# Kernel tuning notes

Hardware: AMD Instinct MI355X
Metric: run time of the kernel (lower is better)

The kernel has to match this reference:

```python
import jax, jax.numpy as jnp
import numpy as np

I3 = jnp.eye(3, dtype=jnp.float32)
G_VEC = jnp.array([0.0, 0.0, -9.80665], dtype=jnp.float32)
# Q diag: [cov_omega x3, cov_acc x3, cov_b_omega x3, cov_b_acc x3, cov_Rot_c_i x3, cov_t_c_i x3]
Q_DIAG = jnp.array([1e-3] * 3 + [1e-2] * 3 + [6e-9] * 3 + [2e-4] * 3 + [1e-9] * 3 + [1e-9] * 3, dtype=jnp.float32)
N_NORM_ROT = 100
N_NORM_ROT_CI = 1000


def skew(v):
    z = jnp.zeros_like(v[0])
    return jnp.stack([jnp.stack([z, -v[2], v[1]]),
                      jnp.stack([v[2], z, -v[0]]),
                      jnp.stack([-v[1], v[0], z])])


def so3exp(phi):
    a2 = jnp.sum(phi * phi)
    small = a2 < 1e-12
    a = jnp.sqrt(jnp.where(small, 1.0, a2))
    axis = phi / a
    c, s = jnp.cos(a), jnp.sin(a)
    big = c * I3 + (1.0 - c) * jnp.outer(axis, axis) + s * skew(axis)
    return jnp.where(small, I3 + skew(phi), big)


def sen3exp(xi):
    # SE_2(3) exponential: xi[:3]=rotation, xi[3:9]=(v, p) parts
    phi = xi[:3]
    a2 = jnp.sum(phi * phi)
    small = a2 < 1e-12
    a = jnp.sqrt(jnp.where(small, 1.0, a2))
    axis = phi / a
    c, s = jnp.cos(a), jnp.sin(a)
    sk = skew(axis)
    R = jnp.where(small, I3 + skew(phi),
                  c * I3 + (1.0 - c) * jnp.outer(axis, axis) + s * sk)
    J = jnp.where(small, I3 + 0.5 * skew(phi),
                  (s / a) * I3 + (1.0 - s / a) * jnp.outer(axis, axis) + ((1.0 - c) / a) * sk)
    x = J @ xi[3:].reshape(2, 3).T  # (3,2): columns are dv, dp
    return R, x


def normalize_rot(R):
    # Polar-factor re-orthonormalization (equivalent to the SVD-based
    # normalize_rot for near-rotation matrices), via Newton-Schulz iteration
    # which is smooth and jit/vjp friendly.
    def body(X, _):
        return 1.5 * X - 0.5 * (X @ X.T @ X), None
    X, _ = jax.lax.scan(body, R, None, length=8)
    return X


def from_rpy(roll, pitch, yaw):
    cr, sr = jnp.cos(roll), jnp.sin(roll)
    cp, sp = jnp.cos(pitch), jnp.sin(pitch)
    cy, sy = jnp.cos(yaw), jnp.sin(yaw)
    one = jnp.ones_like(cr)
    zero = jnp.zeros_like(cr)
    Rx = jnp.stack([jnp.stack([one, zero, zero]), jnp.stack([zero, cr, -sr]), jnp.stack([zero, sr, cr])])
    Ry = jnp.stack([jnp.stack([cp, zero, sp]), jnp.stack([zero, one, zero]), jnp.stack([-sp, zero, cp])])
    Rz = jnp.stack([jnp.stack([cy, -sy, zero]), jnp.stack([sy, cy, zero]), jnp.stack([zero, zero, one])])
    return Rz @ Ry @ Rx


def init_covariance():
    P = jnp.zeros((21, 21), dtype=jnp.float32)
    P = P.at[:2, :2].set(1e-3 * jnp.eye(2))     # cov_Rot0 (no yaw error)
    P = P.at[3:5, 3:5].set(0.1 * jnp.eye(2))    # cov_v0
    P = P.at[9:12, 9:12].set(6e-3 * I3)         # cov_b_omega0
    P = P.at[12:15, 12:15].set(4e-3 * I3)       # cov_b_acc0
    P = P.at[15:18, 15:18].set(1e-6 * I3)       # cov_Rot_c_i0
    P = P.at[18:21, 18:21].set(5e-3 * I3)       # cov_t_c_i0
    return P


def propagate_cov(P, Rot, v, p, dt):
    F = jnp.zeros((21, 21), dtype=P.dtype)
    F = F.at[3:6, :3].set(skew(G_VEC))
    F = F.at[6:9, 3:6].set(I3)
    F = F.at[:3, 9:12].set(-Rot)
    F = F.at[3:6, 9:12].set(-skew(v) @ Rot)
    F = F.at[3:6, 12:15].set(-Rot)
    F = F.at[6:9, 9:12].set(-skew(p) @ Rot)
    G = jnp.zeros((21, 18), dtype=P.dtype)
    G = G.at[:3, :3].set(Rot)
    G = G.at[3:6, 3:6].set(Rot)
    G = G.at[9:12, 6:9].set(I3)
    G = G.at[12:15, 9:12].set(I3)
    G = G.at[15:18, 12:15].set(I3)
    G = G.at[18:21, 15:18].set(I3)
    F = F * dt
    G = G * dt
    F2 = F @ F
    Phi = jnp.eye(21, dtype=P.dtype) + F + 0.5 * F2 + (F2 @ F) / 6.0  # 3rd-order expm
    return Phi @ (P + (G * Q_DIAG[None, :]) @ G.T) @ Phi.T


def _step(carry, xs):
    Rot, v, p, b_om, b_ac, Rci, tci, P = carry
    u_i, dt_i, mcov_i, i = xs
    # ---- propagate ----
    acc = Rot @ (u_i[3:6] - b_ac) + G_VEC
    v_n = v + acc * dt_i
    p_n = p + v * dt_i + 0.5 * acc * dt_i * dt_i
    Rot_n = Rot @ so3exp((u_i[:3] - b_om) * dt_i)
    P_n = propagate_cov(P, Rot, v, p, dt_i)
    # ---- update: zero lateral/vertical body-velocity pseudo-measurement ----
    omega = u_i[:3] - b_om
    Rot_body = Rot_n @ Rci
    v_imu = Rot_n.T @ v_n
    v_body = Rci.T @ v_imu + skew(tci) @ omega
    H = jnp.zeros((2, 21), dtype=P.dtype)
    H = H.at[:, 3:6].set(Rot_body.T[1:])
    H = H.at[:, 15:18].set((Rci.T @ skew(v_imu))[1:])
    H = H.at[:, 9:12].set(skew(tci)[1:])
    H = H.at[:, 18:21].set(-skew(omega)[1:])
    r = -v_body[1:]
    Rm = jnp.diag(mcov_i)
    S = H @ P_n @ H.T + Rm                    # (2,2)
    K = jnp.linalg.solve(S, H @ P_n).T        # K = P H^T S^-1 (P, S symmetric)
    dx = K @ r                                 # (21,)
    dR, dxi = sen3exp(dx[:9])
    Rot_u = dR @ Rot_n
    v_u = dR @ v_n + dxi[:, 0]
    p_u = dR @ p_n + dxi[:, 1]
    b_om_u = b_om + dx[9:12]
    b_ac_u = b_ac + dx[12:15]
    Rci_u = so3exp(dx[15:18]) @ Rci
    tci_u = tci + dx[18:21]
    IKH = jnp.eye(21, dtype=P.dtype) - K @ H
    P_u = IKH @ P_n @ IKH.T + K @ Rm @ K.T    # Joseph form
    P_u = 0.5 * (P_u + P_u.T)
    Rot_u = jnp.where(i % N_NORM_ROT == 0, normalize_rot(Rot_u), Rot_u)
    Rci_u = jnp.where(i % N_NORM_ROT_CI == 0, normalize_rot(Rci_u), Rci_u)
    carry = (Rot_u, v_u, p_u, b_om_u, b_ac_u, Rci_u, tci_u, P_u)
    return carry, (Rot_u, v_u, p_u, b_om_u, b_ac_u, Rci_u, tci_u)


def _forward(t, u, measurements_covs, v_mes, p_mes, ang0, N):
    dt = t[1:N] - t[:N - 1]
    Rot0 = from_rpy(ang0[0], ang0[1], ang0[2])
    z3 = jnp.zeros(3, dtype=u.dtype)
    carry0 = (Rot0, v_mes[0], z3, z3, z3, I3, z3, init_covariance())
    xs = (u[1:N], dt, measurements_covs[1:N], jnp.arange(1, N))
    _, ys = jax.lax.scan(_step, carry0, xs)
    Rot = jnp.concatenate([Rot0[None], ys[0]], axis=0)
    v = jnp.concatenate([v_mes[0][None], ys[1]], axis=0)
    p = jnp.concatenate([z3[None], ys[2]], axis=0)
    b_omega = jnp.concatenate([z3[None], ys[3]], axis=0)
    b_acc = jnp.concatenate([z3[None], ys[4]], axis=0)
    Rot_c_i = jnp.concatenate([I3[None], ys[5]], axis=0)
    t_c_i = jnp.concatenate([z3[None], ys[6]], axis=0)
    return (Rot, v, p, b_omega, b_acc, Rot_c_i, t_c_i)


def setup_inputs() -> dict:
    key = jax.random.key(0)
    N = 20000  # 200 s at 100 Hz IMU
    k0, k1, k2, k3, k4, k5 = jax.random.split(key, 6)
    t = jnp.arange(N, dtype=jnp.float32) * 0.01
    gyro = 0.01 * jax.random.normal(k0, (N, 3), dtype=jnp.float32)
    acc = jnp.array([0.0, 0.0, 9.80665], jnp.float32) + 0.1 * jax.random.normal(k1, (N, 3), dtype=jnp.float32)
    u = jnp.concatenate([gyro, acc], axis=1)
    measurements_covs = 0.1 + jax.random.uniform(k2, (N, 2), dtype=jnp.float32)
    v_mes = jax.random.normal(k3, (N, 3), dtype=jnp.float32)
    p_mes = jax.random.normal(k4, (N, 3), dtype=jnp.float32)
    ang0 = 0.01 * jax.random.normal(k5, (3,), dtype=jnp.float32)
    return dict(t=t, u=u, measurements_covs=measurements_covs, v_mes=v_mes, p_mes=p_mes, ang0=ang0, N=N)


def reference(t, u, measurements_covs, v_mes, p_mes, ang0, N):
    return _forward(t, u, measurements_covs, v_mes, p_mes, ang0, N)
```

## Files before the change

### kernel.cpp

```cpp
#include <hip/hip_runtime.h>

#define GRAV 9.80665f
#define WAVE_SYNC() do { \
    asm volatile("s_waitcnt lgkmcnt(0)" ::: "memory"); \
    __builtin_amdgcn_sched_barrier(0); \
  } while(0)

#define LDP 28

__device__ __forceinline__ float sel3(int r, float a0, float a1, float a2){
  float x = (r==1)? a1 : a0;
  return (r>=2)? a2 : x;
}
__device__ __forceinline__ float RL(float v, int k){
  return __int_as_float(__builtin_amdgcn_readlane(__float_as_int(v), k));
}
__device__ __forceinline__ float pick9(int k, const float* X){
  float s=X[0];
  s=(k==1)?X[1]:s; s=(k==2)?X[2]:s; s=(k==3)?X[3]:s; s=(k==4)?X[4]:s;
  s=(k==5)?X[5]:s; s=(k==6)?X[6]:s; s=(k==7)?X[7]:s; s=(k==8)?X[8]:s;
  return s;
}

__device__ __forceinline__ void mm33(float* __restrict__ O, const float* A, const float* B){
#pragma unroll
  for(int r=0;r<3;++r){
#pragma unroll
    for(int c=0;c<3;++c){
      O[r*3+c] = A[r*3+0]*B[0*3+c] + A[r*3+1]*B[1*3+c] + A[r*3+2]*B[2*3+c];
    }
  }
}

__device__ __forceinline__ void rot_from_t2(float t_, float p0, float p1, float p2, float* R){
  float c_, k1_, k2_;
  if (t_ < 1e-4f){
    c_  = 1.f - t_*(0.5f - t_*((1.f/24.f) - t_*(1.f/720.f)));
    k2_ = 1.f - t_*((1.f/6.f) - t_*((1.f/120.f) - t_*(1.f/5040.f)));
    k1_ = 0.5f - t_*((1.f/24.f) - t_*(1.f/720.f));
  } else {
    float a = sqrtf(t_);
    c_ = __cosf(a);
    float s = __sinf(a);
    k2_ = s/a;
    k1_ = (1.f - c_)/t_;
  }
  R[0]=c_+k1_*p0*p0;      R[1]=k1_*p0*p1-k2_*p2;  R[2]=k1_*p0*p2+k2_*p1;
  R[3]=k1_*p0*p1+k2_*p2;  R[4]=c_+k1_*p1*p1;      R[5]=k1_*p1*p2-k2_*p0;
  R[6]=k1_*p0*p2-k2_*p1;  R[7]=k1_*p1*p2+k2_*p0;  R[8]=c_+k1_*p2*p2;
}

__device__ __forceinline__ void normalize_rot9(float* X){
#pragma unroll 1
  for(int it=0; it<8; ++it){
    float Y[9], Z[9];
#pragma unroll
    for(int r=0;r<3;++r)
#pragma unroll
      for(int c=0;c<3;++c)
        Y[r*3+c] = X[r*3+0]*X[c*3+0] + X[r*3+1]*X[c*3+1] + X[r*3+2]*X[c*3+2];
#pragma unroll
    for(int r=0;r<3;++r)
#pragma unroll
      for(int c=0;c<3;++c)
        Z[r*3+c] = Y[r*3+0]*X[0*3+c] + Y[r*3+1]*X[1*3+c] + Y[r*3+2]*X[2*3+c];
#pragma unroll
    for(int e=0;e<9;++e) X[e] = 1.5f*X[e] - 0.5f*Z[e];
  }
}

__device__ __forceinline__ float pick_state(int l,
    const float* Rt, const float* vv, const float* pp,
    const float* bw, const float* ba, const float* Rc, const float* tc){
  float s = Rt[0];
  s=(l==1)?Rt[1]:s;  s=(l==2)?Rt[2]:s;  s=(l==3)?Rt[3]:s;  s=(l==4)?Rt[4]:s;
  s=(l==5)?Rt[5]:s;  s=(l==6)?Rt[6]:s;  s=(l==7)?Rt[7]:s;  s=(l==8)?Rt[8]:s;
  s=(l==9)?vv[0]:s;  s=(l==10)?vv[1]:s; s=(l==11)?vv[2]:s;
  s=(l==12)?pp[0]:s; s=(l==13)?pp[1]:s; s=(l==14)?pp[2]:s;
  s=(l==15)?bw[0]:s; s=(l==16)?bw[1]:s; s=(l==17)?bw[2]:s;
  s=(l==18)?ba[0]:s; s=(l==19)?ba[1]:s; s=(l==20)?ba[2]:s;
  s=(l==21)?Rc[0]:s; s=(l==22)?Rc[1]:s; s=(l==23)?Rc[2]:s;
  s=(l==24)?Rc[3]:s; s=(l==25)?Rc[4]:s; s=(l==26)?Rc[5]:s;
  s=(l==27)?Rc[6]:s; s=(l==28)?Rc[7]:s; s=(l==29)?Rc[8]:s;
  s=(l==30)?tc[0]:s; s=(l==31)?tc[1]:s; s=(l==32)?tc[2]:s;
  return s;
}

__global__ __launch_bounds__(64,1)
void iekf_scan_kernel(const float* __restrict__ t,
                      const float* __restrict__ u,
                      const float* __restrict__ mcov,
                      const float* __restrict__ v_mes,
                      const float* __restrict__ ang0,
                      float* __restrict__ out, int N)
{
  const int l = threadIdx.x;
  __shared__ __align__(16) float Pm[21*LDP];
  __shared__ __align__(16) float Eb[21*LDP];

  for (int e=l; e<21*LDP; e+=64){
    int r=e/LDP, c=e-(e/LDP)*LDP;
    float vI=0.f;
    if (r==c){
      if (r<2) vI=0.001f;
      else if (r==3||r==4) vI=0.1f;
      else if (r>=9&&r<12) vI=0.006f;
      else if (r>=12&&r<15) vI=0.004f;
      else if (r>=15&&r<18) vI=1e-6f;
      else if (r>=18&&r<21) vI=0.005f;
    }
    Pm[e]=vI;
  }

  int ostr=0; float* op = out;
  {
    int obase=0, ooff=0;
    if (l<9)       {obase=0;    ostr=9; ooff=l;}
    else if (l<12) {obase=9*N;  ostr=3; ooff=l-9;}
    else if (l<15) {obase=12*N; ostr=3; ooff=l-12;}
    else if (l<18) {obase=15*N; ostr=3; ooff=l-15;}
    else if (l<21) {obase=18*N; ostr=3; ooff=l-18;}
    else if (l<30) {obase=21*N; ostr=9; ooff=l-21;}
    else           {obase=30*N; ostr=3; ooff=l-30;}
    op = out + obase + ooff;
  }

  const int g21 = l/21;
  const int c21 = l - g21*21;
  const int cw  = 9 + 4*g21;
  int l1 = l+21; if (l1>=63) l1-=63;
  int l2 = l+42; if (l2>=63) l2-=63;
  static const int cols[12] = {3,4,5, 9,10,11, 15,16,17, 18,19,20};

  float myval = 0.f;
  {
    float Rt0[9], vv0[3], pp0[3], bwa[3], baa[3], Rc0[9], tca[3];
    float rl = ang0[0], pt = ang0[1], yw = ang0[2];
    float cr=cosf(rl), sr=sinf(rl), cp=cosf(pt), sp=sinf(pt), cy=cosf(yw), sy=sinf(yw);
    Rt0[0]=cy*cp; Rt0[1]=cy*sp*sr - sy*cr; Rt0[2]=cy*sp*cr + sy*sr;
    Rt0[3]=sy*cp; Rt0[4]=sy*sp*sr + cy*cr; Rt0[5]=sy*sp*cr - cy*sr;
    Rt0[6]=-sp;   Rt0[7]=cp*sr;            Rt0[8]=cp*cr;
    vv0[0]=v_mes[0]; vv0[1]=v_mes[1]; vv0[2]=v_mes[2];
#pragma unroll
    for(int k=0;k<3;++k){ pp0[k]=0.f; bwa[k]=0.f; baa[k]=0.f; tca[k]=0.f; }
    Rc0[0]=1.f;Rc0[1]=0.f;Rc0[2]=0.f;Rc0[3]=0.f;Rc0[4]=1.f;Rc0[5]=0.f;Rc0[6]=0.f;Rc0[7]=0.f;Rc0[8]=1.f;
    float sv = pick_state(l, Rt0, vv0, pp0, bwa, baa, Rc0, tca);
    if (l<33){ op[0] = sv; myval = sv; }
  }
  WAVE_SYNC();

  float tA = t[0], tB = t[1];
  float cu[6];
#pragma unroll
  for(int k=0;k<6;++k) cu[k]=u[6+k];
  float cm0=mcov[2], cm1=mcov[3];

  int nx100=100, nx1000=1000;

#pragma unroll 1
  for (int i=1; i<N; ++i){
    float dt = tB - tA;
    float u0=cu[0], u1=cu[1], u2=cu[2], u3=cu[3], u4=cu[4], u5=cu[5];
    float crm0=cm0, crm1=cm1;
    if (i+1 < N){
      tA = tB; tB = t[i+1];
#pragma unroll
      for(int k=0;k<6;++k) cu[k]=u[(i+1)*6+k];
      cm0 = mcov[(i+1)*2]; cm1 = mcov[(i+1)*2+1];
    }

    float Rt[9];
#pragma unroll
    for(int k=0;k<9;++k) Rt[k] = RL(myval, k);
    float vv0s=RL(myval,9),  vv1s=RL(myval,10), vv2s=RL(myval,11);
    float pp0s=RL(myval,12), pp1s=RL(myval,13), pp2s=RL(myval,14);
    float bw0=RL(myval,15),  bw1=RL(myval,16),  bw2=RL(myval,17);
    float ba0=RL(myval,18),  ba1=RL(myval,19),  ba2=RL(myval,20);
    float Rc[9];
#pragma unroll
    for(int k=0;k<9;++k) Rc[k] = RL(myval, 21+k);
    float tc0=RL(myval,30), tc1=RL(myval,31), tc2=RL(myval,32);

    float dt2=dt*dt, gdt=GRAV*dt, hdt=0.5f*dt, hdt2=0.5f*dt*dt;
    float hgdt2 = 0.5f*gdt*dt;
    float g6d   = gdt*dt2*(1.0f/6.0f);

    float w0=u0-bw0, w1=u1-bw1, w2=u2-bw2;
    float aa0=u3-ba0, aa1=u4-ba1, aa2=u5-ba2;
    float acc0 = Rt[0]*aa0+Rt[1]*aa1+Rt[2]*aa2;
    float acc1 = Rt[3]*aa0+Rt[4]*aa1+Rt[5]*aa2;
    float acc2 = Rt[6]*aa0+Rt[7]*aa1+Rt[8]*aa2 - GRAV;
    float vn0=vv0s+acc0*dt, vn1=vv1s+acc1*dt, vn2=vv2s+acc2*dt;
    float pn0=pp0s+vv0s*dt+acc0*hdt2;
    float pn1=pp1s+vv1s*dt+acc1*hdt2;
    float pn2=pp2s+vv2s*dt+acc2*hdt2;
    float ph0=w0*dt, ph1=w1*dt, ph2=w2*dt;
    float dRs[9]; rot_from_t2(ph0*ph0+ph1*ph1+ph2*ph2, ph0,ph1,ph2, dRs);
    float Rn[9]; mm33(Rn, Rt, dRs);

    float RtG[3], RtA[3], RtB[3];
#pragma unroll
    for(int k=0;k<3;++k){
      float r0=Rt[k], r3=Rt[3+k], r6=Rt[6+k];
      RtG[k] = sel3(g21, r0, r3, r6);
      RtA[k] = sel3(g21, r3, r6, r0);
      RtB[k] = sel3(g21, r6, r0, r3);
    }
    float vAs = sel3(g21, vv2s, vv0s, vv1s), vBs = sel3(g21, vv1s, vv2s, vv0s);
    float pAs = sel3(g21, pp2s, pp0s, pp1s), pBs = sel3(g21, pp1s, pp2s, pp0s);
    float Bs0,Bs1,Bs2, Cs0,Cs1,Cs2, Ds0,Ds1,Ds2;
    {
      float bs[3], cs[3], ds[3];
#pragma unroll
      for(int k=0;k<3;++k){
        bs[k] = -dt*RtG[k];
        float craw = dt*(vAs*RtA[k] - vBs*RtB[k]);
        float selC = sel3(g21, -RtA[k], RtB[k], 0.f);
        cs[k] = craw + hgdt2*selC;
        float draw = dt*(pAs*RtA[k] - pBs*RtB[k]);
        ds[k] = draw + hdt*craw + g6d*selC;
      }
      Bs0=bs[0];Bs1=bs[1];Bs2=bs[2];
      Cs0=cs[0];Cs1=cs[1];Cs2=cs[2];
      Ds0=ds[0];Ds1=ds[1];Ds2=ds[2];
    }

    float q0d=0.001f*dt2, q1d=0.01f*dt2;
    float q69=6e-9f*dt2, q24=2e-4f*dt2, q19=1e-9f*dt2;

    if (l<63){
      int c = c21;
      const float4* Pr4 = (const float4*)(Pm + c*LDP);
      float4 a0=Pr4[0], a1=Pr4[1], a2=Pr4[2], a3=Pr4[3], a4=Pr4[4];
      float m20 = Pm[c*LDP + 20];

      bool cl3 = (c<3);
      bool c36 = (c>=3 && c<6);
      int csel = c36 ? (c-3) : (cl3 ? c : 0);
      float Rtc0 = sel3(csel, Rt[0], Rt[3], Rt[6]);
      float Rtc1 = sel3(csel, Rt[1], Rt[4], Rt[7]);
      float Rtc2 = sel3(csel, Rt[2], Rt[5], Rt[8]);
      float dot0 = Rt[0]*Rtc0 + Rt[1]*Rtc1 + Rt[2]*Rtc2;
      float dot1 = Rt[3]*Rtc0 + Rt[4]*Rtc1 + Rt[5]*Rtc2;
      float dotg = RtG[0]*Rtc0 + RtG[1]*Rtc1 + RtG[2]*Rtc2;

      float m0  = a0.x + (cl3 ? q0d*dot0 : 0.f);
      float m1  = a0.y + (cl3 ? q0d*dot1 : 0.f);
      float mr  = sel3(g21, a0.x, a0.y, a0.z) + (cl3 ? q0d*dotg : 0.f);
      float m3r = sel3(g21, a0.w, a1.x, a1.y) + (c36 ? q1d*dotg : 0.f);
      float m6r = sel3(g21, a1.z, a1.w, a2.x);
      float m9  = a2.y + ((c==9) ? q69 : 0.f);
      float m10 = a2.z + ((c==10)? q69 : 0.f);
      float m11 = a2.w + ((c==11)? q69 : 0.f);
      float m12 = a3.x + ((c==12)? q24 : 0.f);
      float m13 = a3.y + ((c==13)? q24 : 0.f);
      float m14 = a3.z + ((c==14)? q24 : 0.f);

      float Ar = (g21==0)? gdt*m1 : (g21==1)? -gdt*m0 : 0.f;
      float bterm = Bs0*m12+Bs1*m13+Bs2*m14;
      float e0 = mr + Bs0*m9+Bs1*m10+Bs2*m11;
      float e1 = m3r + Ar + Cs0*m9+Cs1*m10+Cs2*m11 + bterm;
      float e2 = m6r + hdt*Ar + dt*m3r + Ds0*m9+Ds1*m10+Ds2*m11 + hdt*bterm;
      Eb[g21*LDP+c]=e0; Eb[(3+g21)*LDP+c]=e1; Eb[(6+g21)*LDP+c]=e2;

      float mc0 = sel3(g21, a2.y, a3.y, a4.y);
      float mc1 = sel3(g21, a2.z, a3.z, a4.z);
      float mc2 = sel3(g21, a2.w, a3.w, a4.w);
      float mc3 = sel3(g21, a3.x, a4.x, m20);
      float qd0 = sel3(g21, q69, q24, q19);
      float qd1 = sel3(g21, q69, q24, q19);
      float qd2 = sel3(g21, q69, q19, q19);
      float qd3 = sel3(g21, q24, q19, q19);
      Eb[(cw+0)*LDP+c] = mc0 + ((cw+0==c)? qd0 : 0.f);
      Eb[(cw+1)*LDP+c] = mc1 + ((cw+1==c)? qd1 : 0.f);
      Eb[(cw+2)*LDP+c] = mc2 + ((cw+2==c)? qd2 : 0.f);
      Eb[(cw+3)*LDP+c] = mc3 + ((cw+3==c)? qd3 : 0.f);
    }

    float H0[12], H1[12];
    float rr0, rr1;
    {
      float Rb1 = Rn[0]*Rc[1]+Rn[1]*Rc[4]+Rn[2]*Rc[7];
      float Rb4 = Rn[3]*Rc[1]+Rn[4]*Rc[4]+Rn[5]*Rc[7];
      float Rb7 = Rn[6]*Rc[1]+Rn[7]*Rc[4]+Rn[8]*Rc[7];
      float Rb2 = Rn[0]*Rc[2]+Rn[1]*Rc[5]+Rn[2]*Rc[8];
      float Rb5 = Rn[3]*Rc[2]+Rn[4]*Rc[5]+Rn[5]*Rc[8];
      float Rb8 = Rn[6]*Rc[2]+Rn[7]*Rc[5]+Rn[8]*Rc[8];
      float vi0 = Rn[0]*vn0+Rn[3]*vn1+Rn[6]*vn2;
      float vi1 = Rn[1]*vn0+Rn[4]*vn1+Rn[7]*vn2;
      float vi2 = Rn[2]*vn0+Rn[5]*vn1+Rn[8]*vn2;
      float vb1 = Rc[1]*vi0+Rc[4]*vi1+Rc[7]*vi2 + (tc2*w0 - tc0*w2);
      float vb2 = Rc[2]*vi0+Rc[5]*vi1+Rc[8]*vi2 + (tc0*w1 - tc1*w0);
      rr0 = -vb1; rr1 = -vb2;
      H0[0]=Rb1; H0[1]=Rb4; H0[2]=Rb7;
      H1[0]=Rb2; H1[1]=Rb5; H1[2]=Rb8;
      H0[3]=tc2;  H0[4]=0.f;  H0[5]=-tc0;
      H1[3]=-tc1; H1[4]=tc0;  H1[5]=0.f;
      H0[6]=Rc[4]*vi2 - Rc[7]*vi1;  H0[7]=Rc[7]*vi0 - Rc[1]*vi2;  H0[8]=Rc[1]*vi1 - Rc[4]*vi0;
      H1[6]=Rc[5]*vi2 - Rc[8]*vi1;  H1[7]=Rc[8]*vi0 - Rc[2]*vi2;  H1[8]=Rc[2]*vi1 - Rc[5]*vi0;
      H0[9]=-w2; H0[10]=0.f; H0[11]=w0;
      H1[9]=w1;  H1[10]=-w0; H1[11]=0.f;
    }
    WAVE_SYNC();

    float pnv[7];
#pragma unroll
    for(int k=0;k<7;++k) pnv[k]=0.f;
    float p0=0.f, p1=0.f;
    if (l<63){
      int r = c21;
      const float4* Er4 = (const float4*)(Eb + r*LDP);
      float4 a0=Er4[0], a1=Er4[1], a2=Er4[2], a3=Er4[3], a4=Er4[4];
      float e20 = Eb[r*LDP + 20];

      float e0a=a0.x, e1a=a0.y;
      float eg  = sel3(g21, a0.x, a0.y, a0.z);
      float e3g = sel3(g21, a0.w, a1.x, a1.y);
      float e6g = sel3(g21, a1.z, a1.w, a2.x);
      float e9=a2.y, e10=a2.z, e11=a2.w, e12=a3.x, e13=a3.y, e14=a3.z;

      float Ag = (g21==0)? gdt*e1a : (g21==1)? -gdt*e0a : 0.f;
      float bterm = Bs0*e12+Bs1*e13+Bs2*e14;
      pnv[0] = eg + Bs0*e9+Bs1*e10+Bs2*e11;
      pnv[1] = e3g + Ag + Cs0*e9+Cs1*e10+Cs2*e11 + bterm;
      pnv[2] = e6g + hdt*Ag + dt*e3g + Ds0*e9+Ds1*e10+Ds2*e11 + hdt*bterm;
      pnv[3] = sel3(g21, a2.y, a3.y, a4.y);
      pnv[4] = sel3(g21, a2.z, a3.z, a4.z);
      pnv[5] = sel3(g21, a2.w, a3.w, a4.w);
      pnv[6] = sel3(g21, a3.x, a4.x, e20);

      float c1a = sel3(g21, H0[0], H0[1], H0[2]);
      float c3a = sel3(g21, H0[3], 0.f,   H0[8]);
      float c4a = sel3(g21, H0[4], 0.f,   H0[9]);
      float c5a = sel3(g21, H0[5], H0[6], H0[10]);
      float c6a = sel3(g21, 0.f,   H0[7], H0[11]);
      float c1b = sel3(g21, H1[0], H1[1], H1[2]);
      float c3b = sel3(g21, H1[3], 0.f,   H1[8]);
      float c4b = sel3(g21, H1[4], 0.f,   H1[9]);
      float c5b = sel3(g21, H1[5], H1[6], H1[10]);
      float c6b = sel3(g21, 0.f,   H1[7], H1[11]);
      p0 = c1a*pnv[1] + c3a*pnv[3] + c4a*pnv[4] + c5a*pnv[5] + c6a*pnv[6];
      p1 = c1b*pnv[1] + c3b*pnv[3] + c4b*pnv[4] + c5b*pnv[5] + c6b*pnv[6];
    }
    float hpr0 = p0 + __shfl(p0, l1) + __shfl(p0, l2);
    float hpr1 = p1 + __shfl(p1, l1) + __shfl(p1, l2);

    float hpjx[7], hpjy[7];
#pragma unroll
    for (int s=0;s<7;++s){
      int j = (s<3)? (g21 + 3*s) : (cw + (s-3));
      hpjx[s] = __shfl(hpr0, j);
      hpjy[s] = __shfl(hpr1, j);
    }

    float hph00=0.f, hph01=0.f, hph10=0.f, hph11=0.f;
#pragma unroll
    for(int k=0;k<12;++k){
      float hp0 = RL(hpr0, cols[k]);
      float hp1 = RL(hpr1, cols[k]);
      hph00 += hp0*H0[k]; hph01 += hp0*H1[k];
      hph10 += hp1*H0[k]; hph11 += hp1*H1[k];
    }
    float s00 = hph00 + crm0, s01 = hph01, s10 = hph10, s11 = hph11 + crm1;
    float idet = 1.0f/(s00*s11 - s01*s10);
    float i00 =  s11*idet, i01 = -s01*idet, i10 = -s10*idet, i11 = s00*idet;
    float K0 = i00*hpr0 + i01*hpr1;
    float K1 = i10*hpr0 + i11*hpr1;
    float s01q = 0.5f*(s01 + s10);
    float dxval = K0*rr0 + K1*rr1;

    float dx0 = RL(dxval,0), dx1 = RL(dxval,1), dx2 = RL(dxval,2);
    float dx3 = RL(dxval,3), dx4 = RL(dxval,4), dx5 = RL(dxval,5);
    float dx6 = RL(dxval,6), dx7 = RL(dxval,7), dx8 = RL(dxval,8);
    float dx15 = RL(dxval,15), dx16 = RL(dxval,16), dx17 = RL(dxval,17);
    int src = (l>=30 && l<33)? (l-12) : ((l>=15 && l<21)? (l-6) : 0);
    float dxadd = __shfl(dxval, src);

    if (l<63){
      int r = c21;
#pragma unroll
      for (int s=0;s<7;++s){
        int j = (s<3)? (g21 + 3*s) : (cw + (s-3));
        float kjx = i00*hpjx[s] + i01*hpjy[s];
        float kjy = i10*hpjx[s] + i11*hpjy[s];
        float cross = (K0*hpjx[s] + K1*hpjy[s]) + (kjx*hpr0 + kjy*hpr1);
        float quad  = (K0*kjx)*s00 + (K0*kjy + K1*kjx)*s01q + (K1*kjy)*s11;
        float val = pnv[s] - cross + quad;
        if (r <= j){
          Pm[r*LDP+j] = val;
          if (r < j) Pm[j*LDP+r] = val;
        }
      }
    }

    float t2x = dx0*dx0+dx1*dx1+dx2*dx2;
    float cX,k1X,k2X,j1X;
    if (t2x < 1e-4f){
      cX  = 1.f - t2x*(0.5f - t2x*((1.f/24.f) - t2x*(1.f/720.f)));
      k2X = 1.f - t2x*((1.f/6.f) - t2x*((1.f/120.f) - t2x*(1.f/5040.f)));
      k1X = 0.5f - t2x*((1.f/24.f) - t2x*(1.f/720.f));
      j1X = (1.f/6.f) - t2x*((1.f/120.f) - t2x*(1.f/5040.f));
    } else {
      float a = sqrtf(t2x);
      cX = __cosf(a);
      float s = __sinf(a);
      k2X = s/a; k1X = (1.f-cX)/t2x; j1X = (1.f-k2X)/t2x;
    }
    float dR[9];
    dR[0]=cX+k1X*dx0*dx0;      dR[1]=k1X*dx0*dx1-k2X*dx2; dR[2]=k1X*dx0*dx2+k2X*dx1;
    dR[3]=k1X*dx0*dx1+k2X*dx2; dR[4]=cX+k1X*dx1*dx1;      dR[5]=k1X*dx1*dx2-k2X*dx0;
    dR[6]=k1X*dx0*dx2-k2X*dx1; dR[7]=k1X*dx1*dx2+k2X*dx0; dR[8]=cX+k1X*dx2*dx2;
    float Jm[9];
    Jm[0]=k2X+j1X*dx0*dx0;      Jm[1]=j1X*dx0*dx1-k1X*dx2; Jm[2]=j1X*dx0*dx2+k1X*dx1;
    Jm[3]=j1X*dx0*dx1+k1X*dx2;  Jm[4]=k2X+j1X*dx1*dx1;     Jm[5]=j1X*dx1*dx2-k1X*dx0;
    Jm[6]=j1X*dx0*dx2-k1X*dx1;  Jm[7]=j1X*dx1*dx2+k1X*dx0; Jm[8]=k2X+j1X*dx2*dx2;
    float Ec[9];
    rot_from_t2(dx15*dx15+dx16*dx16+dx17*dx17, dx15,dx16,dx17, Ec);

    float nv = 0.f;
    if (l<9){
      int ro=(l>=6)?2:((l>=3)?1:0); int co=l-3*ro;
      float d0=sel3(ro,dR[0],dR[3],dR[6]), d1=sel3(ro,dR[1],dR[4],dR[7]), d2=sel3(ro,dR[2],dR[5],dR[8]);
      float n0=sel3(co,Rn[0],Rn[1],Rn[2]), n1=sel3(co,Rn[3],Rn[4],Rn[5]), n2=sel3(co,Rn[6],Rn[7],Rn[8]);
      nv = d0*n0 + d1*n1 + d2*n2;
    } else if (l<15){
      int j=l-9; bool isv=(j<3); int ro = isv? j : (j-3);
      float x0 = isv? vn0:pn0, x1 = isv? vn1:pn1, x2 = isv? vn2:pn2;
      float y0 = isv? dx3:dx6, y1 = isv? dx4:dx7, y2 = isv? dx5:dx8;
      float d0=sel3(ro,dR[0],dR[3],dR[6]), d1=sel3(ro,dR[1],dR[4],dR[7]), d2=sel3(ro,dR[2],dR[5],dR[8]);
      float j0=sel3(ro,Jm[0],Jm[3],Jm[6]), j1m=sel3(ro,Jm[1],Jm[4],Jm[7]), j2m=sel3(ro,Jm[2],Jm[5],Jm[8]);
      nv = d0*x0 + d1*x1 + d2*x2 + j0*y0 + j1m*y1 + j2m*y2;
    } else if (l<21){
      float old = (l<18)? sel3(l-15,bw0,bw1,bw2) : sel3(l-18,ba0,ba1,ba2);
      nv = old + dxadd;
    } else if (l<30){
      int j=l-21; int ro=(j>=6)?2:((j>=3)?1:0); int co=j-3*ro;
      float e0=sel3(ro,Ec[0],Ec[3],Ec[6]), e1=sel3(ro,Ec[1],Ec[4],Ec[7]), e2=sel3(ro,Ec[2],Ec[5],Ec[8]);
      float r0=sel3(co,Rc[0],Rc[1],Rc[2]), r1=sel3(co,Rc[3],Rc[4],Rc[5]), r2=sel3(co,Rc[6],Rc[7],Rc[8]);
      nv = e0*r0 + e1*r1 + e2*r2;
    } else if (l<33){
      nv = sel3(l-30,tc0,tc1,tc2) + dxadd;
    }
    if (l<33) myval = nv;

    bool n100 = (i==nx100), n1000 = (i==nx1000);
    if (n100) nx100 += 100;
    if (n1000) nx1000 += 1000;
    if (n100 || n1000){
      if (n100){
        float X[9];
#pragma unroll
        for (int k=0;k<9;++k) X[k]=RL(myval,k);
        normalize_rot9(X);
        if (l<9) myval = pick9(l,X);
      }
      if (n1000){
        float Y[9];
#pragma unroll
        for (int k=0;k<9;++k) Y[k]=RL(myval,21+k);
        normalize_rot9(Y);
        if (l>=21 && l<30) myval = pick9(l-21,Y);
      }
    }

    if (l<33) op[i*ostr] = myval;

    WAVE_SYNC();
  }
}

extern "C" void kernel_launch(void* const* d_in, const int* in_sizes, int n_in,
                              void* d_out, int out_size, void* d_ws, size_t ws_size,
                              hipStream_t stream) {
  (void)n_in; (void)out_size; (void)d_ws; (void)ws_size;
  const float* t     = (const float*)d_in[0];
  const float* u     = (const float*)d_in[1];
  const float* mcov  = (const float*)d_in[2];
  const float* v_mes = (const float*)d_in[3];
  const float* ang0  = (const float*)d_in[5];
  int N = in_sizes[0];
  iekf_scan_kernel<<<dim3(1), dim3(64), 0, stream>>>(t, u, mcov, v_mes, ang0, (float*)d_out, N);
}
```

Baseline: 49.86 ms.

## Restructure IEKF step to update in pre-propagation frame and defer covariance propagation

Reformulates the per-step filter so the Kalman update uses the pre-propagation covariance held in registers (Mr) with H composed with the propagation Jacobian (G), and moves the covariance propagation after the state update. The persistent P matrix in shared memory becomes a per-lane register slice plus a symmetrizing transpose through a scratch buffer. The aim is to shorten the serial dependency chain per step, since the state update no longer waits on the full F P F^T pass through shared memory. In exchange it adds a 21-wide readlane broadcast, extra shuffles and a symmetrization pass, and small numerical differences are possible.

```diff
diff --git a/kernel.cpp b/kernel.cpp
--- a/kernel.cpp
+++ b/kernel.cpp
@@ -95,22 +95,8 @@
                       float* __restrict__ out, int N)
 {
   const int l = threadIdx.x;
-  __shared__ __align__(16) float Pm[21*LDP];
   __shared__ __align__(16) float Eb[21*LDP];
-
-  for (int e=l; e<21*LDP; e+=64){
-    int r=e/LDP, c=e-(e/LDP)*LDP;
-    float vI=0.f;
-    if (r==c){
-      if (r<2) vI=0.001f;
-      else if (r==3||r==4) vI=0.1f;
-      else if (r>=9&&r<12) vI=0.006f;
-      else if (r>=12&&r<15) vI=0.004f;
-      else if (r>=15&&r<18) vI=1e-6f;
-      else if (r>=18&&r<21) vI=0.005f;
-    }
-    Pm[e]=vI;
-  }
+  __shared__ __align__(16) float PnS[21*LDP];
 
   int ostr=0; float* op = out;
   {
@@ -130,7 +116,6 @@
   const int cw  = 9 + 4*g21;
   int l1 = l+21; if (l1>=63) l1-=63;
   int l2 = l+42; if (l2>=63) l2-=63;
-  static const int cols[12] = {3,4,5, 9,10,11, 15,16,17, 18,19,20};
 
   float myval = 0.f;
   {
@@ -147,7 +132,23 @@
     float sv = pick_state(l, Rt0, vv0, pp0, bwa, baa, Rc0, tca);
     if (l<33){ op[0] = sv; myval = sv; }
   }
-  WAVE_SYNC();
+
+  float Mr[7];
+  {
+    int r = c21;
+    float dv = 0.f;
+    if (r<2) dv=0.001f;
+    else if (r==3||r==4) dv=0.1f;
+    else if (r>=9&&r<12) dv=0.006f;
+    else if (r>=12&&r<15) dv=0.004f;
+    else if (r>=15&&r<18) dv=1e-6f;
+    else if (r>=18&&r<21) dv=0.005f;
+#pragma unroll
+    for (int s=0;s<7;++s){
+      int j = (s<3)? (g21 + 3*s) : (cw + (s-3));
+      Mr[s] = (j==c21)? dv : 0.f;
+    }
+  }
 
   float tA = t[0], tB = t[1];
   float cu[6];
@@ -182,8 +183,36 @@
     float tc0=RL(myval,30), tc1=RL(myval,31), tc2=RL(myval,32);
 
     float dt2=dt*dt, gdt=GRAV*dt, hdt=0.5f*dt, hdt2=0.5f*dt*dt;
-    float hgdt2 = 0.5f*gdt*dt;
-    float g6d   = gdt*dt2*(1.0f/6.0f);
+    float g6 = gdt*dt*(1.0f/6.0f);
+    float q0d=0.001f*dt2, q1d=0.01f*dt2;
+    float q69=6e-9f*dt2, q24=2e-4f*dt2, q19=1e-9f*dt2;
+
+    float RRT00=Rt[0]*Rt[0]+Rt[1]*Rt[1]+Rt[2]*Rt[2];
+    float RRT01=Rt[0]*Rt[3]+Rt[1]*Rt[4]+Rt[2]*Rt[5];
+    float RRT02=Rt[0]*Rt[6]+Rt[1]*Rt[7]+Rt[2]*Rt[8];
+    float RRT11=Rt[3]*Rt[3]+Rt[4]*Rt[4]+Rt[5]*Rt[5];
+    float RRT12=Rt[3]*Rt[6]+Rt[4]*Rt[7]+Rt[5]*Rt[8];
+    float RRT22=Rt[6]*Rt[6]+Rt[7]*Rt[7]+Rt[8]*Rt[8];
+    {
+      int r = c21;
+      float rr_a = sel3(r, RRT00, RRT01, RRT02);
+      float rr_b = sel3(r, RRT01, RRT11, RRT12);
+      float rr_c = sel3(r, RRT02, RRT12, RRT22);
+      if (r<3) Mr[0] += q0d * sel3(g21, rr_a, rr_b, rr_c);
+      int rm = r-3;
+      float r2a = sel3(rm, RRT00, RRT01, RRT02);
+      float r2b = sel3(rm, RRT01, RRT11, RRT12);
+      float r2c = sel3(rm, RRT02, RRT12, RRT22);
+      if (r>=3 && r<6) Mr[1] += q1d * sel3(g21, r2a, r2b, r2c);
+      float qd3 = sel3(g21, q69, q24, q19);
+      float qd4 = sel3(g21, q69, q24, q19);
+      float qd5 = sel3(g21, q69, q19, q19);
+      float qd6 = sel3(g21, q24, q19, q19);
+      if (cw   == r) Mr[3] += qd3;
+      if (cw+1 == r) Mr[4] += qd4;
+      if (cw+2 == r) Mr[5] += qd5;
+      if (cw+3 == r) Mr[6] += qd6;
+    }
 
     float w0=u0-bw0, w1=u1-bw1, w2=u2-bw2;
     float aa0=u3-ba0, aa1=u4-ba1, aa2=u5-ba2;
@@ -197,85 +226,6 @@
     float ph0=w0*dt, ph1=w1*dt, ph2=w2*dt;
     float dRs[9]; rot_from_t2(ph0*ph0+ph1*ph1+ph2*ph2, ph0,ph1,ph2, dRs);
     float Rn[9]; mm33(Rn, Rt, dRs);
-
-    float RtG[3], RtA[3], RtB[3];
-#pragma unroll
-    for(int k=0;k<3;++k){
-      float r0=Rt[k], r3=Rt[3+k], r6=Rt[6+k];
-      RtG[k] = sel3(g21, r0, r3, r6);
-      RtA[k] = sel3(g21, r3, r6, r0);
-      RtB[k] = sel3(g21, r6, r0, r3);
-    }
-    float vAs = sel3(g21, vv2s, vv0s, vv1s), vBs = sel3(g21, vv1s, vv2s, vv0s);
-    float pAs = sel3(g21, pp2s, pp0s, pp1s), pBs = sel3(g21, pp1s, pp2s, pp0s);
-    float Bs0,Bs1,Bs2, Cs0,Cs1,Cs2, Ds0,Ds1,Ds2;
-    {
-      float bs[3], cs[3], ds[3];
-#pragma unroll
-      for(int k=0;k<3;++k){
-        bs[k] = -dt*RtG[k];
-        float craw = dt*(vAs*RtA[k] - vBs*RtB[k]);
-        float selC = sel3(g21, -RtA[k], RtB[k], 0.f);
-        cs[k] = craw + hgdt2*selC;
-        float draw = dt*(pAs*RtA[k] - pBs*RtB[k]);
-        ds[k] = draw + hdt*craw + g6d*selC;
-      }
-      Bs0=bs[0];Bs1=bs[1];Bs2=bs[2];
-      Cs0=cs[0];Cs1=cs[1];Cs2=cs[2];
-      Ds0=ds[0];Ds1=ds[1];Ds2=ds[2];
-    }
-
-    float q0d=0.001f*dt2, q1d=0.01f*dt2;
-    float q69=6e-9f*dt2, q24=2e-4f*dt2, q19=1e-9f*dt2;
-
-    if (l<63){
-      int c = c21;
-      const float4* Pr4 = (const float4*)(Pm + c*LDP);
-      float4 a0=Pr4[0], a1=Pr4[1], a2=Pr4[2], a3=Pr4[3], a4=Pr4[4];
-      float m20 = Pm[c*LDP + 20];
-
-      bool cl3 = (c<3);
-      bool c36 = (c>=3 && c<6);
-      int csel = c36 ? (c-3) : (cl3 ? c : 0);
-      float Rtc0 = sel3(csel, Rt[0], Rt[3], Rt[6]);
-      float Rtc1 = sel3(csel, Rt[1], Rt[4], Rt[7]);
-      float Rtc2 = sel3(csel, Rt[2], Rt[5], Rt[8]);
-      float dot0 = Rt[0]*Rtc0 + Rt[1]*Rtc1 + Rt[2]*Rtc2;
-      float dot1 = Rt[3]*Rtc0 + Rt[4]*Rtc1 + Rt[5]*Rtc2;
-      float dotg = RtG[0]*Rtc0 + RtG[1]*Rtc1 + RtG[2]*Rtc2;
-
-      float m0  = a0.x + (cl3 ? q0d*dot0 : 0.f);
-      float m1  = a0.y + (cl3 ? q0d*dot1 : 0.f);
-      float mr  = sel3(g21, a0.x, a0.y, a0.z) + (cl3 ? q0d*dotg : 0.f);
-      float m3r = sel3(g21, a0.w, a1.x, a1.y) + (c36 ? q1d*dotg : 0.f);
-      float m6r = sel3(g21, a1.z, a1.w, a2.x);
-      float m9  = a2.y + ((c==9) ? q69 : 0.f);
-      float m10 = a2.z + ((c==10)? q69 : 0.f);
-      float m11 = a2.w + ((c==11)? q69 : 0.f);
-      float m12 = a3.x + ((c==12)? q24 : 0.f);
-      float m13 = a3.y + ((c==13)? q24 : 0.f);
-      float m14 = a3.z + ((c==14)? q24 : 0.f);
-
-      float Ar = (g21==0)? gdt*m1 : (g21==1)? -gdt*m0 : 0.f;
-      float bterm = Bs0*m12+Bs1*m13+Bs2*m14;
-      float e0 = mr + Bs0*m9+Bs1*m10+Bs2*m11;
-      float e1 = m3r + Ar + Cs0*m9+Cs1*m10+Cs2*m11 + bterm;
-      float e2 = m6r + hdt*Ar + dt*m3r + Ds0*m9+Ds1*m10+Ds2*m11 + hdt*bterm;
-      Eb[g21*LDP+c]=e0; Eb[(3+g21)*LDP+c]=e1; Eb[(6+g21)*LDP+c]=e2;
-
-      float mc0 = sel3(g21, a2.y, a3.y, a4.y);
-      float mc1 = sel3(g21, a2.z, a3.z, a4.z);
-      float mc2 = sel3(g21, a2.w, a3.w, a4.w);
-      float mc3 = sel3(g21, a3.x, a4.x, m20);
-      float qd0 = sel3(g21, q69, q24, q19);
-      float qd1 = sel3(g21, q69, q24, q19);
-      float qd2 = sel3(g21, q69, q19, q19);
-      float qd3 = sel3(g21, q24, q19, q19);
-      Eb[(cw+0)*LDP+c] = mc0 + ((cw+0==c)? qd0 : 0.f);
-      Eb[(cw+1)*LDP+c] = mc1 + ((cw+1==c)? qd1 : 0.f);
-      Eb[(cw+2)*LDP+c] = mc2 + ((cw+2==c)? qd2 : 0.f);
-      Eb[(cw+3)*LDP+c] = mc3 + ((cw+3==c)? qd3 : 0.f);
-    }
 
     float H0[12], H1[12];
     float rr0, rr1;
@@ -301,96 +251,144 @@
       H0[9]=-w2; H0[10]=0.f; H0[11]=w0;
       H1[9]=w1;  H1[10]=-w0; H1[11]=0.f;
     }
-    WAVE_SYNC();
-
-    float pnv[7];
-#pragma unroll
-    for(int k=0;k<7;++k) pnv[k]=0.f;
-    float p0=0.f, p1=0.f;
-    if (l<63){
-      int r = c21;
-      const float4* Er4 = (const float4*)(Eb + r*LDP);
-      float4 a0=Er4[0], a1=Er4[1], a2=Er4[2], a3=Er4[3], a4=Er4[4];
-      float e20 = Eb[r*LDP + 20];
-
-      float e0a=a0.x, e1a=a0.y;
-      float eg  = sel3(g21, a0.x, a0.y, a0.z);
-      float e3g = sel3(g21, a0.w, a1.x, a1.y);
-      float e6g = sel3(g21, a1.z, a1.w, a2.x);
-      float e9=a2.y, e10=a2.z, e11=a2.w, e12=a3.x, e13=a3.y, e14=a3.z;
-
-      float Ag = (g21==0)? gdt*e1a : (g21==1)? -gdt*e0a : 0.f;
-      float bterm = Bs0*e12+Bs1*e13+Bs2*e14;
-      pnv[0] = eg + Bs0*e9+Bs1*e10+Bs2*e11;
-      pnv[1] = e3g + Ag + Cs0*e9+Cs1*e10+Cs2*e11 + bterm;
-      pnv[2] = e6g + hdt*Ag + dt*e3g + Ds0*e9+Ds1*e10+Ds2*e11 + hdt*bterm;
-      pnv[3] = sel3(g21, a2.y, a3.y, a4.y);
-      pnv[4] = sel3(g21, a2.z, a3.z, a4.z);
-      pnv[5] = sel3(g21, a2.w, a3.w, a4.w);
-      pnv[6] = sel3(g21, a3.x, a4.x, e20);
-
-      float c1a = sel3(g21, H0[0], H0[1], H0[2]);
-      float c3a = sel3(g21, H0[3], 0.f,   H0[8]);
-      float c4a = sel3(g21, H0[4], 0.f,   H0[9]);
-      float c5a = sel3(g21, H0[5], H0[6], H0[10]);
-      float c6a = sel3(g21, 0.f,   H0[7], H0[11]);
-      float c1b = sel3(g21, H1[0], H1[1], H1[2]);
-      float c3b = sel3(g21, H1[3], 0.f,   H1[8]);
-      float c4b = sel3(g21, H1[4], 0.f,   H1[9]);
-      float c5b = sel3(g21, H1[5], H1[6], H1[10]);
-      float c6b = sel3(g21, 0.f,   H1[7], H1[11]);
-      p0 = c1a*pnv[1] + c3a*pnv[3] + c4a*pnv[4] + c5a*pnv[5] + c6a*pnv[6];
-      p1 = c1b*pnv[1] + c3b*pnv[3] + c4b*pnv[4] + c5b*pnv[5] + c6b*pnv[6];
-    }
-    float hpr0 = p0 + __shfl(p0, l1) + __shfl(p0, l2);
-    float hpr1 = p1 + __shfl(p1, l1) + __shfl(p1, l2);
-
-    float hpjx[7], hpjy[7];
-#pragma unroll
-    for (int s=0;s<7;++s){
-      int j = (s<3)? (g21 + 3*s) : (cw + (s-3));
-      hpjx[s] = __shfl(hpr0, j);
-      hpjy[s] = __shfl(hpr1, j);
-    }
-
-    float hph00=0.f, hph01=0.f, hph10=0.f, hph11=0.f;
-#pragma unroll
-    for(int k=0;k<12;++k){
-      float hp0 = RL(hpr0, cols[k]);
-      float hp1 = RL(hpr1, cols[k]);
-      hph00 += hp0*H0[k]; hph01 += hp0*H1[k];
-      hph10 += hp1*H0[k]; hph11 += hp1*H1[k];
-    }
-    float s00 = hph00 + crm0, s01 = hph01, s10 = hph10, s11 = hph11 + crm1;
+
+    float Bm[9], Cab[9], D2a[9];
+#pragma unroll
+    for(int k=0;k<3;++k){
+      float b0=-dt*Rt[k], b1=-dt*Rt[3+k], b2=-dt*Rt[6+k];
+      float c0=dt*(vv2s*Rt[3+k]-vv1s*Rt[6+k]);
+      float c1=dt*(vv0s*Rt[6+k]-vv2s*Rt[k]);
+      float c2=dt*(vv1s*Rt[k]-vv0s*Rt[3+k]);
+      float d0=dt*(pp2s*Rt[3+k]-pp1s*Rt[6+k]);
+      float d1=dt*(pp0s*Rt[6+k]-pp2s*Rt[k]);
+      float d2=dt*(pp1s*Rt[k]-pp0s*Rt[3+k]);
+      Bm[k]=b0; Bm[3+k]=b1; Bm[6+k]=b2;
+      Cab[k]=c0+0.5f*gdt*b1; Cab[3+k]=c1-0.5f*gdt*b0; Cab[6+k]=c2;
+      D2a[k]=d0+hdt*c0+g6*b1; D2a[3+k]=d1+hdt*c1-g6*b0; D2a[6+k]=d2+hdt*c2;
+    }
+
+    float G0_0 = -gdt*H0[1], G1_0 = -gdt*H1[1];
+    float G0_1 =  gdt*H0[0], G1_1 =  gdt*H1[0];
+    float G0_9[3], G1_9[3], G0_12[3], G1_12[3];
+#pragma unroll
+    for(int k=0;k<3;++k){
+      G0_9[k]  = H0[3+k] + H0[0]*Cab[k] + H0[1]*Cab[3+k] + H0[2]*Cab[6+k];
+      G1_9[k]  = H1[3+k] + H1[0]*Cab[k] + H1[1]*Cab[3+k] + H1[2]*Cab[6+k];
+      G0_12[k] = H0[0]*Bm[k] + H0[1]*Bm[3+k] + H0[2]*Bm[6+k];
+      G1_12[k] = H1[0]*Bm[k] + H1[1]*Bm[3+k] + H1[2]*Bm[6+k];
+    }
+
+    float gj0[7], gj1[7];
+    gj0[0] = sel3(g21, G0_0, G0_1, 0.f);   gj1[0] = sel3(g21, G1_0, G1_1, 0.f);
+    gj0[1] = sel3(g21, H0[0], H0[1], H0[2]); gj1[1] = sel3(g21, H1[0], H1[1], H1[2]);
+    gj0[2] = 0.f; gj1[2] = 0.f;
+    gj0[3] = sel3(g21, G0_9[0],  G0_12[1], H0[8]);   gj1[3] = sel3(g21, G1_9[0],  G1_12[1], H1[8]);
+    gj0[4] = sel3(g21, G0_9[1],  G0_12[2], H0[9]);   gj1[4] = sel3(g21, G1_9[1],  G1_12[2], H1[9]);
+    gj0[5] = sel3(g21, G0_9[2],  H0[6],    H0[10]);  gj1[5] = sel3(g21, G1_9[2],  H1[6],    H1[10]);
+    gj0[6] = sel3(g21, G0_12[0], H0[7],    H0[11]);  gj1[6] = sel3(g21, G1_12[0], H1[7],    H1[11]);
+    float pw0=0.f, pw1=0.f;
+#pragma unroll
+    for(int s=0;s<7;++s){ pw0 += Mr[s]*gj0[s]; pw1 += Mr[s]*gj1[s]; }
+    float Wx  = pw0 + __shfl(pw0, l1) + __shfl(pw0, l2);
+    float Wyv = pw1 + __shfl(pw1, l1) + __shfl(pw1, l2);
+
+    float swx[21], swy[21];
+#pragma unroll
+    for(int j=0;j<21;++j){ swx[j] = RL(Wx, j); swy[j] = RL(Wyv, j); }
+
+    float s00=crm0, s01=0.f, s10=0.f, s11=crm1;
+    {
+      s00 += G0_0*swx[0] + G0_1*swx[1];  s01 += G0_0*swy[0] + G0_1*swy[1];
+      s10 += G1_0*swx[0] + G1_1*swx[1];  s11 += G1_0*swy[0] + G1_1*swy[1];
+#pragma unroll
+      for(int k=0;k<3;++k){
+        s00 += H0[k]*swx[3+k];  s01 += H0[k]*swy[3+k];
+        s10 += H1[k]*swx[3+k];  s11 += H1[k]*swy[3+k];
+        s00 += G0_9[k]*swx[9+k];  s01 += G0_9[k]*swy[9+k];
+        s10 += G1_9[k]*swx[9+k];  s11 += G1_9[k]*swy[9+k];
+        s00 += G0_12[k]*swx[12+k]; s01 += G0_12[k]*swy[12+k];
+        s10 += G1_12[k]*swx[12+k]; s11 += G1_12[k]*swy[12+k];
+        s00 += H0[6+k]*swx[15+k]; s01 += H0[6+k]*swy[15+k];
+        s10 += H1[6+k]*swx[15+k]; s11 += H1[6+k]*swy[15+k];
+        s00 += H0[9+k]*swx[18+k]; s01 += H0[9+k]*swy[18+k];
+        s10 += H1[9+k]*swx[18+k]; s11 += H1[9+k]*swy[18+k];
+      }
+    }
     float idet = 1.0f/(s00*s11 - s01*s10);
     float i00 =  s11*idet, i01 = -s01*idet, i10 = -s10*idet, i11 = s00*idet;
-    float K0 = i00*hpr0 + i01*hpr1;
-    float K1 = i10*hpr0 + i11*hpr1;
     float s01q = 0.5f*(s01 + s10);
-    float dxval = K0*rr0 + K1*rr1;
-
-    float dx0 = RL(dxval,0), dx1 = RL(dxval,1), dx2 = RL(dxval,2);
-    float dx3 = RL(dxval,3), dx4 = RL(dxval,4), dx5 = RL(dxval,5);
-    float dx6 = RL(dxval,6), dx7 = RL(dxval,7), dx8 = RL(dxval,8);
-    float dx15 = RL(dxval,15), dx16 = RL(dxval,16), dx17 = RL(dxval,17);
-    int src = (l>=30 && l<33)? (l-12) : ((l>=15 && l<21)? (l-6) : 0);
-    float dxadd = __shfl(dxval, src);
+    float y0 = i00*rr0 + i10*rr1;
+    float y1 = i01*rr0 + i11*rr1;
+
+    float wy[21];
+#pragma unroll
+    for(int j=0;j<21;++j) wy[j] = swx[j]*y0 + swy[j]*y1;
+    float dx0 = wy[0] + Bm[0]*wy[9] + Bm[1]*wy[10] + Bm[2]*wy[11];
+    float dx1 = wy[1] + Bm[3]*wy[9] + Bm[4]*wy[10] + Bm[5]*wy[11];
+    float dx2 = wy[2] + Bm[6]*wy[9] + Bm[7]*wy[10] + Bm[8]*wy[11];
+    float bt0 = Bm[0]*wy[12] + Bm[1]*wy[13] + Bm[2]*wy[14];
+    float bt1 = Bm[3]*wy[12] + Bm[4]*wy[13] + Bm[5]*wy[14];
+    float bt2 = Bm[6]*wy[12] + Bm[7]*wy[13] + Bm[8]*wy[14];
+    float dx3 = wy[3] + gdt*wy[1] + Cab[0]*wy[9]+Cab[1]*wy[10]+Cab[2]*wy[11] + bt0;
+    float dx4 = wy[4] - gdt*wy[0] + Cab[3]*wy[9]+Cab[4]*wy[10]+Cab[5]*wy[11] + bt1;
+    float dx5 = wy[5]             + Cab[6]*wy[9]+Cab[7]*wy[10]+Cab[8]*wy[11] + bt2;
+    float dx6 = wy[6] + dt*wy[3] + hdt*(gdt*wy[1])  + D2a[0]*wy[9]+D2a[1]*wy[10]+D2a[2]*wy[11] + hdt*bt0;
+    float dx7 = wy[7] + dt*wy[4] + hdt*(-gdt*wy[0]) + D2a[3]*wy[9]+D2a[4]*wy[10]+D2a[5]*wy[11] + hdt*bt1;
+    float dx8 = wy[8] + dt*wy[5]                    + D2a[6]*wy[9]+D2a[7]*wy[10]+D2a[8]*wy[11] + hdt*bt2;
+    float dx9 =wy[9],  dx10=wy[10], dx11=wy[11], dx12=wy[12], dx13=wy[13], dx14=wy[14];
+    float dx15=wy[15], dx16=wy[16], dx17=wy[17], dx18=wy[18], dx19=wy[19], dx20=wy[20];
+
+    float Kmx = i00*Wx + i01*Wyv;
+    float Kmy = i10*Wx + i11*Wyv;
+    float mp0,mp1,mp2,mp3,mp4,mp5,mp6;
+    {
+      float sjx[7], sjy[7];
+      sjx[0]=sel3(g21,swx[0],swx[1],swx[2]);   sjy[0]=sel3(g21,swy[0],swy[1],swy[2]);
+      sjx[1]=sel3(g21,swx[3],swx[4],swx[5]);   sjy[1]=sel3(g21,swy[3],swy[4],swy[5]);
+      sjx[2]=sel3(g21,swx[6],swx[7],swx[8]);   sjy[2]=sel3(g21,swy[6],swy[7],swy[8]);
+      sjx[3]=sel3(g21,swx[9],swx[13],swx[17]); sjy[3]=sel3(g21,swy[9],swy[13],swy[17]);
+      sjx[4]=sel3(g21,swx[10],swx[14],swx[18]);sjy[4]=sel3(g21,swy[10],swy[14],swy[18]);
+      sjx[5]=sel3(g21,swx[11],swx[15],swx[19]);sjy[5]=sel3(g21,swy[11],swy[15],swy[19]);
+      sjx[6]=sel3(g21,swx[12],swx[16],swx[20]);sjy[6]=sel3(g21,swy[12],swy[16],swy[20]);
+      float mpo[7];
+#pragma unroll
+      for(int s=0;s<7;++s){
+        float kjx = i00*sjx[s] + i01*sjy[s];
+        float kjy = i10*sjx[s] + i11*sjy[s];
+        float cross = (Kmx*sjx[s] + Kmy*sjy[s]) + (kjx*Wx + kjy*Wyv);
+        float quad  = (Kmx*kjx)*s00 + (Kmx*kjy + Kmy*kjx)*s01q + (Kmy*kjy)*s11;
+        mpo[s] = Mr[s] - cross + quad;
+      }
+      mp0=mpo[0]; mp1=mpo[1]; mp2=mpo[2]; mp3=mpo[3]; mp4=mpo[4]; mp5=mpo[5]; mp6=mpo[6];
+    }
+
+    float mb0  = __shfl(mp0, c21);
+    float mb1  = __shfl(mp0, 21+c21);
+    float mb9  = __shfl(mp3, c21);
+    float mb10 = __shfl(mp4, c21);
+    float mb11 = __shfl(mp5, c21);
+    float mb12 = __shfl(mp6, c21);
+    float mb13 = __shfl(mp3, 21+c21);
+    float mb14 = __shfl(mp4, 21+c21);
+
+    float Bs0=sel3(g21,Bm[0],Bm[3],Bm[6]),  Bs1=sel3(g21,Bm[1],Bm[4],Bm[7]),  Bs2=sel3(g21,Bm[2],Bm[5],Bm[8]);
+    float Cs0=sel3(g21,Cab[0],Cab[3],Cab[6]),Cs1=sel3(g21,Cab[1],Cab[4],Cab[7]),Cs2=sel3(g21,Cab[2],Cab[5],Cab[8]);
+    float Ds0=sel3(g21,D2a[0],D2a[3],D2a[6]),Ds1=sel3(g21,D2a[1],D2a[4],D2a[7]),Ds2=sel3(g21,D2a[2],D2a[5],D2a[8]);
 
     if (l<63){
-      int r = c21;
-#pragma unroll
-      for (int s=0;s<7;++s){
-        int j = (s<3)? (g21 + 3*s) : (cw + (s-3));
-        float kjx = i00*hpjx[s] + i01*hpjy[s];
-        float kjy = i10*hpjx[s] + i11*hpjy[s];
-        float cross = (K0*hpjx[s] + K1*hpjy[s]) + (kjx*hpr0 + kjy*hpr1);
-        float quad  = (K0*kjx)*s00 + (K0*kjy + K1*kjx)*s01q + (K1*kjy)*s11;
-        float val = pnv[s] - cross + quad;
-        if (r <= j){
-          Pm[r*LDP+j] = val;
-          if (r < j) Pm[j*LDP+r] = val;
-        }
-      }
+      int c = c21;
+      float Ar2 = (g21==0)? gdt*mb1 : (g21==1)? -gdt*mb0 : 0.f;
+      float bterm = Bs0*mb12 + Bs1*mb13 + Bs2*mb14;
+      float e0 = mp0 + Bs0*mb9 + Bs1*mb10 + Bs2*mb11;
+      float e1 = mp1 + Ar2 + Cs0*mb9 + Cs1*mb10 + Cs2*mb11 + bterm;
+      float e2 = mp2 + hdt*Ar2 + dt*mp1 + Ds0*mb9 + Ds1*mb10 + Ds2*mb11 + hdt*bterm;
+      Eb[g21*LDP+c]     = e0;
+      Eb[(3+g21)*LDP+c] = e1;
+      Eb[(6+g21)*LDP+c] = e2;
+      Eb[(cw+0)*LDP+c] = mp3;
+      Eb[(cw+1)*LDP+c] = mp4;
+      Eb[(cw+2)*LDP+c] = mp5;
+      Eb[(cw+3)*LDP+c] = mp6;
     }
 
     float t2x = dx0*dx0+dx1*dx1+dx2*dx2;
@@ -426,22 +424,59 @@
     } else if (l<15){
       int j=l-9; bool isv=(j<3); int ro = isv? j : (j-3);
       float x0 = isv? vn0:pn0, x1 = isv? vn1:pn1, x2 = isv? vn2:pn2;
-      float y0 = isv? dx3:dx6, y1 = isv? dx4:dx7, y2 = isv? dx5:dx8;
+      float y0b = isv? dx3:dx6, y1b = isv? dx4:dx7, y2b = isv? dx5:dx8;
       float d0=sel3(ro,dR[0],dR[3],dR[6]), d1=sel3(ro,dR[1],dR[4],dR[7]), d2=sel3(ro,dR[2],dR[5],dR[8]);
       float j0=sel3(ro,Jm[0],Jm[3],Jm[6]), j1m=sel3(ro,Jm[1],Jm[4],Jm[7]), j2m=sel3(ro,Jm[2],Jm[5],Jm[8]);
-      nv = d0*x0 + d1*x1 + d2*x2 + j0*y0 + j1m*y1 + j2m*y2;
+      nv = d0*x0 + d1*x1 + d2*x2 + j0*y0b + j1m*y1b + j2m*y2b;
     } else if (l<21){
       float old = (l<18)? sel3(l-15,bw0,bw1,bw2) : sel3(l-18,ba0,ba1,ba2);
-      nv = old + dxadd;
+      float add = (l<18)? sel3(l-15,dx9,dx10,dx11) : sel3(l-18,dx12,dx13,dx14);
+      nv = old + add;
     } else if (l<30){
       int j=l-21; int ro=(j>=6)?2:((j>=3)?1:0); int co=j-3*ro;
       float e0=sel3(ro,Ec[0],Ec[3],Ec[6]), e1=sel3(ro,Ec[1],Ec[4],Ec[7]), e2=sel3(ro,Ec[2],Ec[5],Ec[8]);
       float r0=sel3(co,Rc[0],Rc[1],Rc[2]), r1=sel3(co,Rc[3],Rc[4],Rc[5]), r2=sel3(co,Rc[6],Rc[7],Rc[8]);
       nv = e0*r0 + e1*r1 + e2*r2;
     } else if (l<33){
-      nv = sel3(l-30,tc0,tc1,tc2) + dxadd;
+      nv = sel3(l-30,tc0,tc1,tc2) + sel3(l-30,dx18,dx19,dx20);
     }
     if (l<33) myval = nv;
+
+    WAVE_SYNC();
+
+    float pnv[7];
+#pragma unroll
+    for(int k=0;k<7;++k) pnv[k]=0.f;
+    if (l<63){
+      int r = c21;
+      const float4* Er4 = (const float4*)(Eb + r*LDP);
+      float4 a0=Er4[0], a1=Er4[1], a2=Er4[2], a3=Er4[3], a4=Er4[4];
+      float e20 = Eb[r*LDP + 20];
+
+      float e0a=a0.x, e1a=a0.y;
+      float eg  = sel3(g21, a0.x, a0.y, a0.z);
+      float e3g = sel3(g21, a0.w, a1.x, a1.y);
+      float e6g = sel3(g21, a1.z, a1.w, a2.x);
+      float e9=a2.y, e10=a2.z, e11=a2.w, e12=a3.x, e13=a3.y, e14=a3.z;
+
+      float Ag = (g21==0)? gdt*e1a : (g21==1)? -gdt*e0a : 0.f;
+      float bterm = Bs0*e12+Bs1*e13+Bs2*e14;
+      pnv[0] = eg + Bs0*e9+Bs1*e10+Bs2*e11;
+      pnv[1] = e3g + Ag + Cs0*e9+Cs1*e10+Cs2*e11 + bterm;
+      pnv[2] = e6g + hdt*Ag + dt*e3g + Ds0*e9+Ds1*e10+Ds2*e11 + hdt*bterm;
+      pnv[3] = sel3(g21, a2.y, a3.y, a4.y);
+      pnv[4] = sel3(g21, a2.z, a3.z, a4.z);
+      pnv[5] = sel3(g21, a2.w, a3.w, a4.w);
+      pnv[6] = sel3(g21, a3.x, a4.x, e20);
+
+      PnS[r*LDP + g21]   = pnv[0];
+      PnS[r*LDP + 3+g21] = pnv[1];
+      PnS[r*LDP + 6+g21] = pnv[2];
+      PnS[r*LDP + cw]    = pnv[3];
+      PnS[r*LDP + cw+1]  = pnv[4];
+      PnS[r*LDP + cw+2]  = pnv[5];
+      PnS[r*LDP + cw+3]  = pnv[6];
+    }
 
     bool n100 = (i==nx100), n1000 = (i==nx1000);
     if (n100) nx100 += 100;
@@ -462,10 +497,19 @@
         if (l>=21 && l<30) myval = pick9(l-21,Y);
       }
     }
-
     if (l<33) op[i*ostr] = myval;
 
     WAVE_SYNC();
+
+    if (l<63){
+      int r = c21;
+#pragma unroll
+      for (int s=0;s<7;++s){
+        int j = (s<3)? (g21 + 3*s) : (cw + (s-3));
+        float pnT = PnS[j*LDP + r];
+        Mr[s] = 0.5f*(pnv[s] + pnT);
+      }
+    }
   }
 }
 
```

New measurement: 59.58 ms. +19.5%, slower.
